# Optimization experiments

Measured on AMD Instinct MI355X. Metric: run time of the kernel, lower is better.

Reference implementation:

```python
import jax, jax.numpy as jnp
import numpy as np

B, H, K, E = 8, 256, 256, 128
VOCAB, FVOCAB = 30000, 1000


def setup_inputs() -> dict:
    key = jax.random.key(0)
    k1, k2, k3, k4, k5, k6 = jax.random.split(key, 6)
    key_emb = jax.random.normal(k2, (VOCAB, E), dtype=jnp.float32)
    value_emb = jax.random.normal(k3, (FVOCAB, E), dtype=jnp.float32)
    # padding_idx=0 rows are zero
    key_emb = key_emb.at[0].set(0.0)
    value_emb = value_emb.at[0].set(0.0)
    return {
        "hidden": jax.random.normal(k1, (B, H, E), dtype=jnp.float32),
        "key_emb": key_emb,
        "value_emb": value_emb,
        "key_seq": jax.random.randint(k4, (B, K), 0, VOCAB, dtype=jnp.int64) if jax.config.jax_enable_x64 else jax.random.randint(k4, (B, K), 0, VOCAB).astype(jnp.int32),
        "value_seq": jax.random.randint(k5, (B, H, K), 0, FVOCAB).astype(jnp.int32),
        "mask_matrix": jax.random.randint(k6, (B, H, K), 0, 2).astype(jnp.int32),
    }


def reference(hidden, key_emb, value_emb, key_seq, value_seq, mask_matrix):
    scale = jnp.asarray(np.power(E, 0.5), dtype=jnp.float32)
    # embedding gathers (padding_idx=0 -> zero row, enforced in setup)
    k = key_emb[key_seq]            # [B, K, E]
    v = value_emb[value_seq]        # [B, H, K, E]
    # masked exp-normalize attention (manual, not softmax: no max-subtract)
    u = jnp.einsum('bhe,bke->bhk', hidden, k) / scale   # [B, H, K]
    delta = jnp.exp(u) * mask_matrix.astype(jnp.float32)
    p = delta / (jnp.sum(delta, axis=2, keepdims=True) + 1e-10)  # [B, H, K]
    # attention-weighted value aggregation
    o = jnp.einsum('bhk,bhke->bhe', p, v)               # [B, H, E]
    # nonzero-count averaging over H
    aspect_len = jnp.sum(o != 0, axis=1).astype(jnp.float32)     # [B, E]
    avg_o = jnp.sum(o, axis=1) / aspect_len                      # [B, E]
    return avg_o
```

## Files before the change

### kernel.cpp

```cpp
#include <hip/hip_runtime.h>
#include <math.h>

#define BB 8
#define HH 256
#define KK 256
#define EE 128

__global__ __launch_bounds__(256) void kvmn_bh(
    const float* __restrict__ hidden,
    const float* __restrict__ key_emb,
    const float* __restrict__ value_emb,
    const int*   __restrict__ key_seq,
    const int*   __restrict__ value_seq,
    const int*   __restrict__ mask,
    float* __restrict__ o_ws)
{
    __shared__ int    sh_ks[KK];
    __shared__ int    sh_vs[KK];
    __shared__ float  sh_p[KK];
    __shared__ float  sh_wsum[4];
    __shared__ float4 sh_o4[8][32];

    const int bid  = blockIdx.x;
    const int b    = bid >> 8;
    const int h    = bid & 255;
    const int tid  = threadIdx.x;
    const int w    = tid >> 6;
    const int lane = tid & 63;
    const int half = lane >> 5;
    const int sub  = lane & 31;

    sh_ks[tid] = key_seq[b * KK + tid];
    sh_vs[tid] = value_seq[(b * HH + h) * KK + tid];
    const int my_mask = mask[(b * HH + h) * KK + tid];

    const float4 h4 = *(const float4*)&hidden[(size_t)(b * HH + h) * EE + sub * 4];

    __syncthreads();

    const float inv_scale = 0.08838834764831845f;

    #pragma unroll 4
    for (int i = 0; i < 32; ++i) {
        const int    k   = w * 64 + i * 2 + half;
        const int    row = sh_ks[k];
        const float4 kv  = *(const float4*)&key_emb[(size_t)row * EE + sub * 4];
        float partial = kv.x * h4.x + kv.y * h4.y + kv.z * h4.z + kv.w * h4.w;
        partial += __shfl_down(partial, 16, 64);
        partial += __shfl_down(partial, 8, 64);
        partial += __shfl_down(partial, 4, 64);
        partial += __shfl_down(partial, 2, 64);
        partial += __shfl_down(partial, 1, 64);
        if (sub == 0) sh_p[k] = partial * inv_scale;
    }
    __syncthreads();

    const float d = expf(sh_p[tid]) * (float)my_mask;
    float wsum = d;
    #pragma unroll
    for (int off = 32; off > 0; off >>= 1)
        wsum += __shfl_down(wsum, off, 64);
    if (lane == 0) sh_wsum[w] = wsum;
    __syncthreads();
    const float denom = sh_wsum[0] + sh_wsum[1] + sh_wsum[2] + sh_wsum[3];
    const float inv   = 1.0f / (denom + 1e-10f);
    sh_p[tid] = d * inv;
    __syncthreads();

    float4 acc = make_float4(0.f, 0.f, 0.f, 0.f);
    #pragma unroll 4
    for (int i = 0; i < 32; ++i) {
        const int    k   = w * 64 + i * 2 + half;
        const float  p   = sh_p[k];
        const int    row = sh_vs[k];
        const float4 v   = *(const float4*)&value_emb[(size_t)row * EE + sub * 4];
        acc.x += p * v.x;
        acc.y += p * v.y;
        acc.z += p * v.z;
        acc.w += p * v.w;
    }
    sh_o4[w * 2 + half][sub] = acc;
    __syncthreads();

    if (tid < 32) {
        float4 s = sh_o4[0][tid];
        #pragma unroll
        for (int r = 1; r < 8; ++r) {
            const float4 t = sh_o4[r][tid];
            s.x += t.x; s.y += t.y; s.z += t.z; s.w += t.w;
        }
        *(float4*)&o_ws[(size_t)(b * HH + h) * EE + tid * 4] = s;
    }
}

__global__ __launch_bounds__(256) void kvmn_reduce(
    const float* __restrict__ o_ws,
    float* __restrict__ out)
{
    __shared__ float sh_sum[256];
    __shared__ int   sh_cnt[256];

    const int b  = blockIdx.x;
    const int t  = threadIdx.x;
    const int e  = t & 127;
    const int hh = t >> 7;

    float sum = 0.0f;
    int   cnt = 0;
    const float* base = o_ws + (size_t)(b * HH + hh * 128) * EE + e;
    #pragma unroll 8
    for (int h = 0; h < 128; ++h) {
        const float v = base[(size_t)h * EE];
        sum += v;
        cnt += (v != 0.0f) ? 1 : 0;
    }
    sh_sum[t] = sum;
    sh_cnt[t] = cnt;
    __syncthreads();
    if (t < 128) {
        const float s = sh_sum[t] + sh_sum[t + 128];
        const int   c = sh_cnt[t] + sh_cnt[t + 128];
        out[b * EE + t] = s / (float)c;
    }
}

__global__ __launch_bounds__(256) void kvmn_final_fb(
    const float* __restrict__ sum_ws, const int* __restrict__ cnt_ws,
    float* __restrict__ out)
{
    const int i = blockIdx.x * blockDim.x + threadIdx.x;
    if (i < BB * EE) out[i] = sum_ws[i] / (float)cnt_ws[i];
}

extern "C" void kernel_launch(void* const* d_in, const int* in_sizes, int n_in,
                              void* d_out, int out_size, void* d_ws, size_t ws_size,
                              hipStream_t stream) {
    const float* hidden    = (const float*)d_in[0];
    const float* key_emb   = (const float*)d_in[1];
    const float* value_emb = (const float*)d_in[2];
    const int*   key_seq   = (const int*)d_in[3];
    const int*   value_seq = (const int*)d_in[4];
    const int*   mask      = (const int*)d_in[5];

    const size_t need = (size_t)BB * HH * EE * sizeof(float);
    float* o_ws = (float*)d_ws;

    kvmn_bh<<<BB * HH, 256, 0, stream>>>(hidden, key_emb, value_emb,
                                         key_seq, value_seq, mask, o_ws);
    kvmn_reduce<<<BB, 256, 0, stream>>>(o_ws, (float*)d_out);
    (void)need; (void)ws_size; (void)in_sizes; (void)n_in; (void)out_size;
}
```

Measured before the change: 105.6 us.

## Split attention into score and aggregation kernels, reuse key rows across 4 heads

```diff
diff --git a/kernel.cpp b/kernel.cpp
--- a/kernel.cpp
+++ b/kernel.cpp
@@ -5,20 +5,96 @@
 #define HH 256
 #define KK 256
 #define EE 128
+#define HG 4
+#define HT (HH / HG)
 
-__global__ __launch_bounds__(256) void kvmn_bh(
+template <int CTRL, int RM>
+__device__ __forceinline__ float dpp_add(float x) {
+    int d = __builtin_amdgcn_update_dpp(0, __float_as_int(x), CTRL, RM, 0xf, true);
+    return x + __int_as_float(d);
+}
+__device__ __forceinline__ float dpp_reduce_half(float x) {
+    x = dpp_add<0x111, 0xf>(x);
+    x = dpp_add<0x112, 0xf>(x);
+    x = dpp_add<0x114, 0xf>(x);
+    x = dpp_add<0x118, 0xf>(x);
+    x = dpp_add<0x142, 0xa>(x);
+    return x;
+}
+__device__ __forceinline__ float dpp_reduce_wave(float x) {
+    x = dpp_reduce_half(x);
+    x = dpp_add<0x143, 0xc>(x);
+    return x;
+}
+
+__global__ __launch_bounds__(256) void kvmn_p(
     const float* __restrict__ hidden,
     const float* __restrict__ key_emb,
+    const int*   __restrict__ key_seq,
+    const int*   __restrict__ mask,
+    float* __restrict__ p_ws)
+{
+    __shared__ int   sh_ks[KK];
+    __shared__ float sh_u[HG][KK];
+    __shared__ float sh_part[HG][4];
+
+    const int b    = blockIdx.x >> 6;
+    const int h0   = (blockIdx.x & (HT - 1)) * HG;
+    const int tid  = threadIdx.x;
+    const int w    = tid >> 6;
+    const int lane = tid & 63;
+    const int half = lane >> 5;
+    const int sub  = lane & 31;
+
+    sh_ks[tid] = key_seq[b * KK + tid];
+
+    float4 h4[HG];
+    #pragma unroll
+    for (int j = 0; j < HG; ++j)
+        h4[j] = *(const float4*)&hidden[(size_t)(b * HH + h0 + j) * EE + sub * 4];
+
+    __syncthreads();
+
+    const float inv_scale = 0.08838834764831845f;
+
+    #pragma unroll 4
+    for (int i = 0; i < 32; ++i) {
+        const int    k   = w * 64 + i * 2 + half;
+        const int    row = sh_ks[k];
+        const float4 kv  = *(const float4*)&key_emb[(size_t)row * EE + sub * 4];
+        #pragma unroll
+        for (int j = 0; j < HG; ++j) {
+            float part = kv.x * h4[j].x + kv.y * h4[j].y + kv.z * h4[j].z + kv.w * h4[j].w;
+            part = dpp_reduce_half(part);
+            if (sub == 31) sh_u[j][k] = part * inv_scale;
+        }
+    }
+    __syncthreads();
+
+    float d[HG];
+    #pragma unroll
+    for (int j = 0; j < HG; ++j) {
+        const int m = mask[(size_t)(b * HH + h0 + j) * KK + tid];
+        d[j] = expf(sh_u[j][tid]) * (float)m;
+        const float s = dpp_reduce_wave(d[j]);
+        if (lane == 63) sh_part[j][w] = s;
+    }
+    __syncthreads();
+    #pragma unroll
+    for (int j = 0; j < HG; ++j) {
+        const float denom = sh_part[j][0] + sh_part[j][1] + sh_part[j][2] + sh_part[j][3];
+        p_ws[(size_t)(b * HH + h0 + j) * KK + tid] = d[j] * (1.0f / (denom + 1e-10f));
+    }
+}
+
+__global__ __launch_bounds__(256) void kvmn_o(
     const float* __restrict__ value_emb,
-    const int*   __restrict__ key_seq,
     const int*   __restrict__ value_seq,
-    const int*   __restrict__ mask,
+    const float* __restrict__ p_ws,
     float* __restrict__ o_ws)
 {
-    __shared__ int    sh_ks[KK];
+    __shared__ float  sh_p[KK];
     __shared__ int    sh_vs[KK];
-    __shared__ float  sh_p[KK];
-    __shared__ float  sh_wsum[4];
     __shared__ float4 sh_o4[8][32];
 
     const int bid  = blockIdx.x;
@@ -30,45 +106,12 @@
     const int half = lane >> 5;
     const int sub  = lane & 31;
 
-    sh_ks[tid] = key_seq[b * KK + tid];
-    sh_vs[tid] = value_seq[(b * HH + h) * KK + tid];
-    const int my_mask = mask[(b * HH + h) * KK + tid];
-
-    const float4 h4 = *(const float4*)&hidden[(size_t)(b * HH + h) * EE + sub * 4];
-
-    __syncthreads();
-
-    const float inv_scale = 0.08838834764831845f;
-
-    #pragma unroll 4
-    for (int i = 0; i < 32; ++i) {
-        const int    k   = w * 64 + i * 2 + half;
-        const int    row = sh_ks[k];
-        const float4 kv  = *(const float4*)&key_emb[(size_t)row * EE + sub * 4];
-        float partial = kv.x * h4.x + kv.y * h4.y + kv.z * h4.z + kv.w * h4.w;
-        partial += __shfl_down(partial, 16, 64);
-        partial += __shfl_down(partial, 8, 64);
-        partial += __shfl_down(partial, 4, 64);
-        partial += __shfl_down(partial, 2, 64);
-        partial += __shfl_down(partial, 1, 64);
-        if (sub == 0) sh_p[k] = partial * inv_scale;
-    }
-    __syncthreads();
-
-    const float d = expf(sh_p[tid]) * (float)my_mask;
-    float wsum = d;
-    #pragma unroll
-    for (int off = 32; off > 0; off >>= 1)
-        wsum += __shfl_down(wsum, off, 64);
-    if (lane == 0) sh_wsum[w] = wsum;
-    __syncthreads();
-    const float denom = sh_wsum[0] + sh_wsum[1] + sh_wsum[2] + sh_wsum[3];
-    const float inv   = 1.0f / (denom + 1e-10f);
-    sh_p[tid] = d * inv;
+    sh_p[tid]  = p_ws[(size_t)(b * HH + h) * KK + tid];
+    sh_vs[tid] = value_seq[(size_t)(b * HH + h) * KK + tid];
     __syncthreads();
 
     float4 acc = make_float4(0.f, 0.f, 0.f, 0.f);
-    #pragma unroll 4
+    #pragma unroll 8
     for (int i = 0; i < 32; ++i) {
         const int    k   = w * 64 + i * 2 + half;
         const float  p   = sh_p[k];
@@ -124,14 +167,6 @@
     }
 }
 
-__global__ __launch_bounds__(256) void kvmn_final_fb(
-    const float* __restrict__ sum_ws, const int* __restrict__ cnt_ws,
-    float* __restrict__ out)
-{
-    const int i = blockIdx.x * blockDim.x + threadIdx.x;
-    if (i < BB * EE) out[i] = sum_ws[i] / (float)cnt_ws[i];
-}
-
 extern "C" void kernel_launch(void* const* d_in, const int* in_sizes, int n_in,
                               void* d_out, int out_size, void* d_ws, size_t ws_size,
                               hipStream_t stream) {
@@ -142,11 +177,11 @@
     const int*   value_seq = (const int*)d_in[4];
     const int*   mask      = (const int*)d_in[5];
 
-    const size_t need = (size_t)BB * HH * EE * sizeof(float);
-    float* o_ws = (float*)d_ws;
+    float* p_ws = (float*)d_ws;
+    float* o_ws = (float*)((char*)d_ws + (size_t)BB * HH * KK * 4);
 
-    kvmn_bh<<<BB * HH, 256, 0, stream>>>(hidden, key_emb, value_emb,
-                                         key_seq, value_seq, mask, o_ws);
+    kvmn_p<<<BB * HT, 256, 0, stream>>>(hidden, key_emb, key_seq, mask, p_ws);
+    kvmn_o<<<BB * HH, 256, 0, stream>>>(value_emb, value_seq, p_ws, o_ws);
     kvmn_reduce<<<BB, 256, 0, stream>>>(o_ws, (float*)d_out);
-    (void)need; (void)ws_size; (void)in_sizes; (void)n_in; (void)out_size;
+    (void)in_sizes; (void)n_in; (void)out_size; (void)ws_size;
 }
```

Result: slower. 109.3 us (+3.6%).
